# Kernel optimization log

Hardware: AMD Instinct MI355X
Metric: run time of the kernel (lower is better)

The kernel has to match this reference:

```python
import jax, jax.numpy as jnp
import numpy as np

MARGIN = 0.5  # init kwarg: margin=0.5, adaptive_margin=True


def setup_inputs() -> dict:
    key = jax.random.key(0)
    k1, k2 = jax.random.split(key)
    B, D, N_CLASSES = 8192, 128, 128
    return {
        "embeddings": jax.random.normal(k1, (B, D), dtype=jnp.float32),
        "labels": jax.random.randint(k2, (B,), 0, N_CLASSES),
    }


def _distance_matrix(e):
    # add 1e-16 where exactly zero, sqrt, then zero those entries back out.
    dot = e @ e.T                      # [B, B]
    sq = jnp.diagonal(dot)             # [B]
    d2 = jax.nn.relu(sq[None, :] - 2.0 * dot + sq[:, None])
    zmask = (d2 == 0.0).astype(e.dtype)
    return jnp.sqrt(d2 + zmask * 1e-16) * (1.0 - zmask)


def reference(embeddings, labels):
    B = embeddings.shape[0]
    # F.normalize(p=2, dim=1) with eps clamp
    norm = jnp.maximum(jnp.linalg.norm(embeddings, axis=1, keepdims=True), 1e-12)
    e = embeddings / norm
    d = _distance_matrix(e)            # [B, B]

    eq = labels[:, None] == labels[None, :]
    eye = jnp.eye(B, dtype=bool)
    pos_mask = eq & ~eye               # same-label, excluding self
    neg_mask = ~eq                     # different-label (diag auto-excluded)

    BIG = jnp.asarray(1e9, d.dtype)
    hardest_pos = jnp.max(jnp.where(pos_mask, d, -BIG), axis=1)  # [B]
    hardest_neg = jnp.min(jnp.where(neg_mask, d, BIG), axis=1)   # [B]
    valid = pos_mask.any(axis=1) & neg_mask.any(axis=1)

    # torch uses .item() -> margin is a constant w.r.t. autodiff
    adaptive_margin = MARGIN * (1.0 + jax.lax.stop_gradient(hardest_pos))
    per_row = jax.nn.relu(hardest_pos - hardest_neg + adaptive_margin)
    per_row = jnp.where(valid, per_row, 0.0)
    count = jnp.maximum(jnp.sum(valid.astype(d.dtype)), 1.0)
    return jnp.sum(per_row) / count
```

## Files before the change

### kernel.cpp

```cpp
#include <hip/hip_runtime.h>

#define BN   8192
#define DIM  128
#define NCLS 128
#define NBLK 1024
#define NSTR 4

typedef __attribute__((ext_vector_type(8))) short bf16x8;
typedef __attribute__((ext_vector_type(4))) float f32x4;

static __device__ __forceinline__ unsigned short f2bf(float x) {
    union { float f; unsigned u; } c; c.f = x;
    unsigned r = c.u + 0x7FFFu + ((c.u >> 16) & 1u);
    return (unsigned short)(r >> 16);
}

static __device__ __forceinline__ bf16x8 ldb8(const unsigned short* p) {
    return *reinterpret_cast<const bf16x8*>(p);
}

static __device__ __forceinline__ unsigned encf(float f) {
    unsigned u = __float_as_uint(f);
    return (u >> 31) ? ~u : (u | 0x80000000u);
}
static __device__ __forceinline__ float decf(unsigned v) {
    return __uint_as_float((v >> 31) ? (v & 0x7FFFFFFFu) : ~v);
}

static __device__ __forceinline__ void gload_lds16(const unsigned short* g, unsigned short* l) {
    __builtin_amdgcn_global_load_lds(
        (const __attribute__((address_space(1))) unsigned int*)g,
        (__attribute__((address_space(3))) unsigned int*)l, 16, 0, 0);
}

__global__ __launch_bounds__(256) void sort_norm(const float* __restrict__ emb,
                                                 const int* __restrict__ labels,
                                                 unsigned short* __restrict__ ebf,
                                                 int2* __restrict__ se,
                                                 unsigned* __restrict__ hp2,
                                                 unsigned* __restrict__ hn2) {
    const int c   = blockIdx.x;
    const int tid = threadIdx.x;
    __shared__ int slab[BN];
    __shared__ int sl[256], so[256];
    __shared__ int srcrow[512];

#pragma unroll 8
    for (int k = 0; k < 32; ++k) {
        int idx = k * 256 + tid;
        slab[idx] = labels[idx];
    }
    __syncthreads();

    int nl = 0, no = 0;
#pragma unroll 8
    for (int k = 0; k < 32; ++k) {
        int lb = slab[k * 256 + tid];
        nl += (lb < c);
        no += (lb == c);
    }
    sl[tid] = nl; so[tid] = no;
    __syncthreads();
    for (int off = 1; off < 256; off <<= 1) {
        int a1 = 0, a2 = 0;
        if (tid >= off) { a1 = sl[tid - off]; a2 = so[tid - off]; }
        __syncthreads();
        sl[tid] += a1; so[tid] += a2;
        __syncthreads();
    }
    const int offs_c = sl[255];
    const int n_c    = so[255];
    int mypos = so[tid] - no;
    for (int k = 0; k < 32; ++k) {
        int r = k * 256 + tid;
        if (slab[r] == c) srcrow[mypos++] = r;
    }
    __syncthreads();

    const int wave = tid >> 6, lane = tid & 63;
    for (int k = wave; k < n_c; k += 4) {
        int r   = srcrow[k];
        int pos = offs_c + k;
        float2 v = reinterpret_cast<const float2*>(emb + (size_t)r * DIM)[lane];
        float ss = v.x * v.x + v.y * v.y;
#pragma unroll
        for (int m = 1; m < 64; m <<= 1) ss += __shfl_xor(ss, m);
        float inv = 1.0f / fmaxf(sqrtf(ss), 1e-12f);
        ushort2 bv; bv.x = f2bf(v.x * inv); bv.y = f2bf(v.y * inv);
        reinterpret_cast<ushort2*>(ebf + (size_t)pos * DIM)[lane] = bv;
        if (lane == 0) {
            se[pos]  = make_int2(offs_c, offs_c + n_c);
            hp2[pos] = 0xFFFFFFFFu;
            hn2[pos] = 0u;
        }
    }
}

__global__ __launch_bounds__(256) void tri_main(const unsigned short* __restrict__ ebf,
                                                const int2* __restrict__ se,
                                                unsigned* __restrict__ hp2,
                                                unsigned* __restrict__ hn2) {
    __shared__ alignas(16) unsigned short as_[2][64 * DIM];

    const int tid  = threadIdx.x;
    const int wave = tid >> 6;
    const int lane = tid & 63;
    const int lr   = lane & 15;
    const int lk   = lane >> 4;
    const int jb   = blockIdx.x >> 5;
    const int isp  = blockIdx.x & 31;
    const int jc0  = jb * 256 + wave * 64;
    const int rb0  = isp * 256;

    bf16x8 b[4][4];
#pragma unroll
    for (int cs = 0; cs < 4; ++cs)
#pragma unroll
        for (int kk = 0; kk < 4; ++kk)
            b[cs][kk] = ldb8(ebf + (size_t)(jc0 + cs * 16 + lr) * DIM + kk * 32 + lk * 8);

    int qs[4], qe[4];
#pragma unroll
    for (int cs = 0; cs < 4; ++cs) {
        int2 q = se[jc0 + cs * 16 + lr];
        qs[cs] = q.x; qe[cs] = q.y;
    }

    float hp[4] = {1e30f, 1e30f, 1e30f, 1e30f};
    float hn[4] = {-1e30f, -1e30f, -1e30f, -1e30f};

    int perm[4];
#pragma unroll
    for (int kk = 0; kk < 4; ++kk) perm[kk] = ((kk * 4 + lk) ^ (lr & 7)) << 4;

    const int rloc  = lane >> 4;
    const int chunk = lane & 15;
    auto STAGE = [&](int buf, int s) {
        const unsigned short* g0 = ebf + (size_t)(rb0 + s * 64) * DIM;
        unsigned short* lb = &as_[buf][wave * 16 * DIM];
#pragma unroll
        for (int l = 0; l < 4; ++l) {
            const int row = l * 4 + rloc;
            gload_lds16(g0 + (size_t)(wave * 16 + row) * DIM + ((chunk ^ (row & 7)) * 8),
                        lb + l * 4 * DIM);
        }
    };

    STAGE(0, 0);
    __syncthreads();

    for (int s = 0; s < NSTR; ++s) {
        if (s < NSTR - 1) STAGE((s + 1) & 1, s + 1);

        const char* bb = reinterpret_cast<const char*>(&as_[s & 1][0]);
        f32x4 acc[4][4];
#pragma unroll
        for (int cs = 0; cs < 4; ++cs)
#pragma unroll
            for (int t = 0; t < 4; ++t) acc[cs][t] = f32x4{0.f, 0.f, 0.f, 0.f};

#pragma unroll
        for (int t = 0; t < 4; ++t)
#pragma unroll
            for (int kk = 0; kk < 4; ++kk) {
                bf16x8 af = *reinterpret_cast<const bf16x8*>(bb + (t * 16 + lr) * 256 + perm[kk]);
                acc[0][t] = __builtin_amdgcn_mfma_f32_16x16x32_bf16(af, b[0][kk], acc[0][t], 0, 0, 0);
                acc[1][t] = __builtin_amdgcn_mfma_f32_16x16x32_bf16(af, b[1][kk], acc[1][t], 0, 0, 0);
                acc[2][t] = __builtin_amdgcn_mfma_f32_16x16x32_bf16(af, b[2][kk], acc[2][t], 0, 0, 0);
                acc[3][t] = __builtin_amdgcn_mfma_f32_16x16x32_bf16(af, b[3][kk], acc[3][t], 0, 0, 0);
            }

        const int rb = rb0 + s * 64;
        bool mixed = false;
#pragma unroll
        for (int cs = 0; cs < 4; ++cs)
            mixed |= (qs[cs] < rb + 64) && (qe[cs] > rb);

        if (!__any(mixed)) {
#pragma unroll
            for (int cs = 0; cs < 4; ++cs) {
                float mx = hn[cs];
#pragma unroll
                for (int t = 0; t < 4; ++t)
#pragma unroll
                    for (int m = 0; m < 4; ++m) mx = fmaxf(mx, acc[cs][t][m]);
                hn[cs] = mx;
            }
        } else {
#pragma unroll
            for (int cs = 0; cs < 4; ++cs)
#pragma unroll
                for (int t = 0; t < 4; ++t)
#pragma unroll
                    for (int m = 0; m < 4; ++m) {
                        const int rowg = rb + t * 16 + lk * 4 + m;
                        const float d = acc[cs][t][m];
                        const bool pos = (rowg >= qs[cs]) && (rowg < qe[cs]);
                        hp[cs] = pos ? fminf(hp[cs], d) : hp[cs];
                        hn[cs] = pos ? hn[cs] : fmaxf(hn[cs], d);
                    }
        }

        __syncthreads();
    }

#pragma unroll
    for (int cs = 0; cs < 4; ++cs) {
#pragma unroll
        for (int sft = 16; sft < 64; sft <<= 1) {
            hp[cs] = fminf(hp[cs], __shfl_xor(hp[cs], sft));
            hn[cs] = fmaxf(hn[cs], __shfl_xor(hn[cs], sft));
        }
    }
    if (lane < 16) {
#pragma unroll
        for (int cs = 0; cs < 4; ++cs) {
            atomicMin(&hp2[jc0 + cs * 16 + lane], encf(hp[cs]));
            atomicMax(&hn2[jc0 + cs * 16 + lane], encf(hn[cs]));
        }
    }
}

__global__ __launch_bounds__(1024) void finalize_kernel(const unsigned* __restrict__ hp2,
                                                        const unsigned* __restrict__ hn2,
                                                        float* __restrict__ out) {
    const int tid = threadIdx.x;
    float sum = 0.f;
#pragma unroll
    for (int it = 0; it < BN / (1024 * 4); ++it) {
        int base = (it * 1024 + tid) * 4;
        uint4 pv = *reinterpret_cast<const uint4*>(&hp2[base]);
        uint4 nv = *reinterpret_cast<const uint4*>(&hn2[base]);
        unsigned pa[4] = {pv.x, pv.y, pv.z, pv.w};
        unsigned na[4] = {nv.x, nv.y, nv.z, nv.w};
#pragma unroll
        for (int e = 0; e < 4; ++e) {
            float pd = decf(pa[e]);
            float nd = decf(na[e]);
            float hpv = sqrtf(fmaxf(2.0f - 2.0f * pd, 0.f));
            float hnv = sqrtf(fmaxf(2.0f - 2.0f * nd, 0.f));
            sum += fmaxf(fmaf(1.5f, hpv, 0.5f) - hnv, 0.f);
        }
    }
    __shared__ float red[1024];
    red[tid] = sum;
    __syncthreads();
    for (int s2 = 512; s2 > 0; s2 >>= 1) {
        if (tid < s2) red[tid] += red[tid + s2];
        __syncthreads();
    }
    if (tid == 0) out[0] = red[0] * (1.0f / (float)BN);
}

extern "C" void kernel_launch(void* const* d_in, const int* in_sizes, int n_in,
                              void* d_out, int out_size, void* d_ws, size_t ws_size,
                              hipStream_t stream) {
    const float* emb    = (const float*)d_in[0];
    const int*   labels = (const int*)d_in[1];
    float* out = (float*)d_out;

    char* ws = (char*)d_ws;
    unsigned short* ebf = (unsigned short*)ws;
    int2*     se   = (int2*)    (ws + 2u * 1024u * 1024u);
    unsigned* hp2  = (unsigned*)(ws + 2u * 1024u * 1024u + 64u * 1024u);
    unsigned* hn2  = (unsigned*)(ws + 2u * 1024u * 1024u + 96u * 1024u);

    hipLaunchKernelGGL(sort_norm,       dim3(NCLS), dim3(256),  0, stream, emb, labels, ebf, se, hp2, hn2);
    hipLaunchKernelGGL(tri_main,        dim3(NBLK), dim3(256),  0, stream, ebf, se, hp2, hn2);
    hipLaunchKernelGGL(finalize_kernel, dim3(1),    dim3(1024), 0, stream, hp2, hn2, out);
}
```

Before: 52.23 us.

## Split label sort into histogram-scan and atomic scatter kernels

Replaces the per-class sort_norm kernel with two kernels. The first is a single-block shared-memory histogram plus prefix scan that produces class offsets. The second normalizes one row per wave across 2048 blocks and scatters each row through a global atomic counter. This removes the redundant full-label scan that each of 128 blocks did before, and spreads normalization over many more blocks. The cost is an extra launch and a within-class row order that is no longer deterministic.

```diff
diff --git a/kernel.cpp b/kernel.cpp
--- a/kernel.cpp
+++ b/kernel.cpp
@@ -33,66 +33,55 @@
         (__attribute__((address_space(3))) unsigned int*)l, 16, 0, 0);
 }
 
-__global__ __launch_bounds__(256) void sort_norm(const float* __restrict__ emb,
-                                                 const int* __restrict__ labels,
-                                                 unsigned short* __restrict__ ebf,
-                                                 int2* __restrict__ se,
-                                                 unsigned* __restrict__ hp2,
-                                                 unsigned* __restrict__ hn2) {
-    const int c   = blockIdx.x;
+__global__ __launch_bounds__(1024) void hist_scan(const int* __restrict__ labels,
+                                                  int* __restrict__ offs,
+                                                  int* __restrict__ cnt) {
+    __shared__ int h[NCLS];
+    __shared__ int sc[NCLS];
     const int tid = threadIdx.x;
-    __shared__ int slab[BN];
-    __shared__ int sl[256], so[256];
-    __shared__ int srcrow[512];
-
-#pragma unroll 8
-    for (int k = 0; k < 32; ++k) {
-        int idx = k * 256 + tid;
-        slab[idx] = labels[idx];
-    }
-    __syncthreads();
-
-    int nl = 0, no = 0;
-#pragma unroll 8
-    for (int k = 0; k < 32; ++k) {
-        int lb = slab[k * 256 + tid];
-        nl += (lb < c);
-        no += (lb == c);
-    }
-    sl[tid] = nl; so[tid] = no;
-    __syncthreads();
-    for (int off = 1; off < 256; off <<= 1) {
-        int a1 = 0, a2 = 0;
-        if (tid >= off) { a1 = sl[tid - off]; a2 = so[tid - off]; }
-        __syncthreads();
-        sl[tid] += a1; so[tid] += a2;
-        __syncthreads();
-    }
-    const int offs_c = sl[255];
-    const int n_c    = so[255];
-    int mypos = so[tid] - no;
-    for (int k = 0; k < 32; ++k) {
-        int r = k * 256 + tid;
-        if (slab[r] == c) srcrow[mypos++] = r;
-    }
-    __syncthreads();
-
-    const int wave = tid >> 6, lane = tid & 63;
-    for (int k = wave; k < n_c; k += 4) {
-        int r   = srcrow[k];
-        int pos = offs_c + k;
-        float2 v = reinterpret_cast<const float2*>(emb + (size_t)r * DIM)[lane];
-        float ss = v.x * v.x + v.y * v.y;
-#pragma unroll
-        for (int m = 1; m < 64; m <<= 1) ss += __shfl_xor(ss, m);
-        float inv = 1.0f / fmaxf(sqrtf(ss), 1e-12f);
-        ushort2 bv; bv.x = f2bf(v.x * inv); bv.y = f2bf(v.y * inv);
-        reinterpret_cast<ushort2*>(ebf + (size_t)pos * DIM)[lane] = bv;
-        if (lane == 0) {
-            se[pos]  = make_int2(offs_c, offs_c + n_c);
-            hp2[pos] = 0xFFFFFFFFu;
-            hn2[pos] = 0u;
-        }
+    if (tid < NCLS) h[tid] = 0;
+    __syncthreads();
+#pragma unroll
+    for (int k = 0; k < BN / 1024; ++k) atomicAdd(&h[labels[k * 1024 + tid]], 1);
+    __syncthreads();
+    int x = 0;
+    if (tid < NCLS) { x = h[tid]; sc[tid] = x; }
+    __syncthreads();
+    for (int off = 1; off < NCLS; off <<= 1) {
+        int v = 0;
+        if (tid < NCLS && tid >= off) v = sc[tid - off];
+        __syncthreads();
+        if (tid < NCLS) sc[tid] += v;
+        __syncthreads();
+    }
+    if (tid < NCLS) { int e = sc[tid] - x; offs[tid] = e; cnt[tid] = e; }
+    if (tid == 0) offs[NCLS] = BN;
+}
+
+__global__ __launch_bounds__(256) void norm_scatter(const float* __restrict__ emb,
+                                                    const int* __restrict__ labels,
+                                                    const int* __restrict__ offs,
+                                                    int* __restrict__ cnt,
+                                                    unsigned short* __restrict__ ebf,
+                                                    int2* __restrict__ se,
+                                                    unsigned* __restrict__ hp2,
+                                                    unsigned* __restrict__ hn2) {
+    const int row  = blockIdx.x * 4 + (threadIdx.x >> 6);
+    const int lane = threadIdx.x & 63;
+    float2 v = reinterpret_cast<const float2*>(emb + (size_t)row * DIM)[lane];
+    float ss = v.x * v.x + v.y * v.y;
+#pragma unroll
+    for (int m = 1; m < 64; m <<= 1) ss += __shfl_xor(ss, m);
+    float inv = 1.0f / fmaxf(sqrtf(ss), 1e-12f);
+    int p = 0, c = 0;
+    if (lane == 0) { c = labels[row]; p = atomicAdd(&cnt[c], 1); }
+    p = __shfl(p, 0); c = __shfl(c, 0);
+    ushort2 bv; bv.x = f2bf(v.x * inv); bv.y = f2bf(v.y * inv);
+    reinterpret_cast<ushort2*>(ebf + (size_t)p * DIM)[lane] = bv;
+    if (lane == 0) {
+        se[p]  = make_int2(offs[c], offs[c + 1]);
+        hp2[p] = 0xFFFFFFFFu;
+        hn2[p] = 0u;
     }
 }
 
@@ -264,8 +253,11 @@
     int2*     se   = (int2*)    (ws + 2u * 1024u * 1024u);
     unsigned* hp2  = (unsigned*)(ws + 2u * 1024u * 1024u + 64u * 1024u);
     unsigned* hn2  = (unsigned*)(ws + 2u * 1024u * 1024u + 96u * 1024u);
-
-    hipLaunchKernelGGL(sort_norm,       dim3(NCLS), dim3(256),  0, stream, emb, labels, ebf, se, hp2, hn2);
-    hipLaunchKernelGGL(tri_main,        dim3(NBLK), dim3(256),  0, stream, ebf, se, hp2, hn2);
-    hipLaunchKernelGGL(finalize_kernel, dim3(1),    dim3(1024), 0, stream, hp2, hn2, out);
-}
+    int*      offs = (int*)     (ws + 2u * 1024u * 1024u + 128u * 1024u);
+    int*      cnt  = (int*)     (ws + 2u * 1024u * 1024u + 130u * 1024u);
+
+    hipLaunchKernelGGL(hist_scan,       dim3(1),      dim3(1024), 0, stream, labels, offs, cnt);
+    hipLaunchKernelGGL(norm_scatter,    dim3(BN / 4), dim3(256),  0, stream, emb, labels, offs, cnt, ebf, se, hp2, hn2);
+    hipLaunchKernelGGL(tri_main,        dim3(NBLK),   dim3(256),  0, stream, ebf, se, hp2, hn2);
+    hipLaunchKernelGGL(finalize_kernel, dim3(1),      dim3(1024), 0, stream, hp2, hn2, out);
+}
```

Measured after the change: 63.19 us. 1.21x slower.
